# Kernel optimization log

Measured on AMD Instinct MI355X. Metric: run time of the kernel, lower is better.

The kernel has to match this reference:

```python
import jax, jax.numpy as jnp
import numpy as np

# Fixed query graph: 3 terms, 3 predicates, edges (head_term, tail_term, pred):
# (0,1,0), (1,2,1), (0,2,2) -> every term has degree 2 -> seq_len 3 incl. self.
T, P, B, D, H, NL, FF = 3, 3, 16384, 256, 8, 2, 1024
DH = D // H
SCALE = DH ** -0.5


def setup_inputs() -> dict:
    key = jax.random.key(0)
    ks = jax.random.split(key, 8)
    s = 0.02
    f = jnp.float32
    return {
        "term_embs": jax.random.normal(ks[0], (T, B, D), f),
        "pred_embs": jax.random.normal(ks[1], (P, B, D), f),
        "Wq": jax.random.normal(ks[2], (NL, D, D), f) * s,
        "Wk": jax.random.normal(ks[3], (NL, D, D), f) * s,
        "Wv": jax.random.normal(ks[4], (NL, D, D), f) * s,
        "Wo": jax.random.normal(ks[5], (NL, D, D), f) * s,
        "bq": jnp.zeros((NL, D), f),
        "bk": jnp.zeros((NL, D), f),
        "bv": jnp.zeros((NL, D), f),
        "bo": jnp.zeros((NL, D), f),
        "ln1_g": jnp.ones((NL, D), f),
        "ln1_b": jnp.zeros((NL, D), f),
        "ln2_g": jnp.ones((NL, D), f),
        "ln2_b": jnp.zeros((NL, D), f),
        "W1": jax.random.normal(ks[6], (NL, D, FF), f) * s,
        "b1": jnp.zeros((NL, FF), f),
        "W2": jax.random.normal(ks[7], (NL, FF, D), f) * s,
        "b2": jnp.zeros((NL, D), f),
        "lnf_g": jnp.ones((D,), f),
        "lnf_b": jnp.zeros((D,), f),
    }


def _layer_norm(x, g, b):
    m = jnp.mean(x, axis=-1, keepdims=True)
    v = jnp.var(x, axis=-1, keepdims=True)
    return (x - m) * jax.lax.rsqrt(v + 1e-5) * g + b


def _forward(term_embs, pred_embs, Wq, Wk, Wv, Wo, bq, bk, bv, bo,
             ln1_g, ln1_b, ln2_g, ln2_b, W1, b1, W2, b2, lnf_g, lnf_b):
    # --- message passing (TransE-style NBP): tail_est = head + pred, head_est = tail - pred
    # edge heads: [0,1,0], edge tails: [1,2,2]
    tail_msgs = term_embs[jnp.array([0, 1, 0])] + pred_embs  # [P,B,D] -> sent to tail terms
    head_msgs = term_embs[jnp.array([1, 2, 2])] - pred_embs  # [P,B,D] -> sent to head terms
    # collect per term (static gather) + self embedding appended last
    x0 = jnp.stack([head_msgs[0], head_msgs[2], term_embs[0]], axis=1)  # [B,3,D]
    x1 = jnp.stack([tail_msgs[0], head_msgs[1], term_embs[1]], axis=1)
    x2 = jnp.stack([tail_msgs[1], tail_msgs[2], term_embs[2]], axis=1)
    x = jnp.concatenate([x0, x1, x2], axis=0)  # [T*B, 3, D]
    # --- pre-norm Transformer encoder, NL layers (dropout off at eval)
    for l in range(NL):
        h = _layer_norm(x, ln1_g[l], ln1_b[l])
        q = (h @ Wq[l] + bq[l]).reshape(-1, 3, H, DH)
        k = (h @ Wk[l] + bk[l]).reshape(-1, 3, H, DH)
        v = (h @ Wv[l] + bv[l]).reshape(-1, 3, H, DH)
        a = jax.nn.softmax(jnp.einsum('nqhd,nkhd->nhqk', q, k) * SCALE, axis=-1)
        o = jnp.einsum('nhqk,nkhd->nqhd', a, v).reshape(-1, 3, D)
        x = x + o @ Wo[l] + bo[l]
        h = _layer_norm(x, ln2_g[l], ln2_b[l])
        x = x + jax.nn.relu(h @ W1[l] + b1[l]) @ W2[l] + b2[l]
    x = _layer_norm(x, lnf_g, lnf_b)
    # --- aggregate (agg_func='mean') over the small message sequence
    return jnp.mean(x, axis=1).reshape(T, B, D)


def reference(term_embs, pred_embs, Wq, Wk, Wv, Wo, bq, bk, bv, bo,
              ln1_g, ln1_b, ln2_g, ln2_b, W1, b1, W2, b2, lnf_g, lnf_b):
    return _forward(term_embs, pred_embs, Wq, Wk, Wv, Wo, bq, bk, bv, bo,
                    ln1_g, ln1_b, ln2_g, ln2_b, W1, b1, W2, b2, lnf_g, lnf_b)
```

## Files before the change

### kernel.cpp

```cpp
#include <hip/hip_runtime.h>
#include <hip/hip_bf16.h>
#include <stdint.h>

typedef __hip_bfloat16 bf16;
typedef unsigned short u16;
typedef unsigned int u32;
typedef __bf16 v8bf __attribute__((ext_vector_type(8)));
typedef float v4f __attribute__((ext_vector_type(4)));

#define NB 16384
#define MROWS 147456

__device__ __forceinline__ float b2f(u16 u) {
  union { u32 u; float f; } v; v.u = ((u32)u) << 16; return v.f;
}
__device__ __forceinline__ u16 f2b(float f) {
  union { float f; u32 u; } v; v.f = f;
  u32 u = v.u;
  return (u16)((u + 0x7fffu + ((u >> 16) & 1u)) >> 16);
}
__device__ __forceinline__ void async16(const u16* g, u16* lds) {
  __builtin_amdgcn_global_load_lds((const __attribute__((address_space(1))) void*)g,
                                   (__attribute__((address_space(3))) void*)lds,
                                   16, 0, 0);
}

__global__ __launch_bounds__(256)
void prep_weights(const float* Wq, const float* Wk, const float* Wv, const float* Wo,
                  const float* W1, const float* W2,
                  const float* bq, const float* bk, const float* bv,
                  bf16* wt, float* bqkv)
{
  if (blockIdx.x == 6144) {
    for (int e = threadIdx.x; e < 1536; e += 256) {
      int l = e / 768;
      int rem = e - l * 768;
      int wsel = rem >> 8;
      int col = rem & 255;
      const float* s = (wsel == 0) ? bq : (wsel == 1) ? bk : bv;
      bqkv[e] = s[l * 256 + col];
    }
    return;
  }
  int gid = blockIdx.x * 256 + threadIdx.x;
  int layer = (gid >= 786432) ? 1 : 0;
  int r = gid - layer * 786432;
  const float* src; int K, N, e, outoff;
  if (r < 262144) {
    int which = r >> 16;
    e = r & 65535; K = 256; N = 256;
    const float* w = (which == 0) ? Wq : (which == 1) ? Wk : (which == 2) ? Wv : Wo;
    src = w + layer * 65536;
    outoff = layer * 786432 + which * 65536;
  } else if (r < 524288) {
    e = r - 262144; K = 256; N = 1024;
    src = W1 + layer * 262144;
    outoff = layer * 786432 + 262144;
  } else {
    e = r - 524288; K = 1024; N = 256;
    src = W2 + layer * 262144;
    outoff = layer * 786432 + 524288;
  }
  int n = e / K, kk = e - n * K;
  ((u16*)wt)[outoff + e] = f2b(src[kk * N + n]);
}

__global__ __launch_bounds__(256)
void build_ln(const float* __restrict__ T, const float* __restrict__ P,
              const float* __restrict__ gp, const float* __restrict__ bp,
              float* __restrict__ X, bf16* __restrict__ H, int row0)
{
  const int lane = threadIdx.x & 63;
  const int lrow = blockIdx.x * 4 + (threadIdx.x >> 6);
  const int row = row0 + lrow;
  const int d0 = lane * 4;
  int n = row / 3;
  int t = row - n * 3;
  float4 v;
  if (t == 2) {
    v = *(const float4*)(T + (size_t)n * 256 + d0);
  } else {
    int tm = n >> 14, b = n & 16383;
    const int srcT[6] = {1, 2,  0, 2,  1, 0};
    const int srcP[6] = {0, 2,  0, 1,  1, 2};
    const float sg[6] = {-1.f, -1.f,  1.f, -1.f,  1.f, 1.f};
    int idx = tm * 2 + t;
    float4 tv = *(const float4*)(T + ((size_t)(srcT[idx] * NB + b)) * 256 + d0);
    float4 pv = *(const float4*)(P + ((size_t)(srcP[idx] * NB + b)) * 256 + d0);
    float s = sg[idx];
    v.x = tv.x + s * pv.x;
    v.y = tv.y + s * pv.y;
    v.z = tv.z + s * pv.z;
    v.w = tv.w + s * pv.w;
  }
  *(float4*)(X + (size_t)lrow * 256 + d0) = v;
  float s = v.x + v.y + v.z + v.w;
  float q = v.x * v.x + v.y * v.y + v.z * v.z + v.w * v.w;
  #pragma unroll
  for (int m = 32; m > 0; m >>= 1) {
    s += __shfl_xor(s, m, 64);
    q += __shfl_xor(q, m, 64);
  }
  float mean = s * (1.f / 256.f);
  float var = q * (1.f / 256.f) - mean * mean;
  float r = rsqrtf(var + 1e-5f);
  float4 gv = *(const float4*)(gp + d0);
  float4 bv = *(const float4*)(bp + d0);
  ushort4 outv;
  outv.x = f2b((v.x - mean) * r * gv.x + bv.x);
  outv.y = f2b((v.y - mean) * r * gv.y + bv.y);
  outv.z = f2b((v.z - mean) * r * gv.z + bv.z);
  outv.w = f2b((v.w - mean) * r * gv.w + bv.w);
  *(ushort4*)((u16*)H + (size_t)lrow * 256 + d0) = outv;
}

__global__ __launch_bounds__(256)
void ln_rows(const float* __restrict__ xp, const float* __restrict__ gp,
             const float* __restrict__ bp, bf16* __restrict__ hp)
{
  const int lane = threadIdx.x & 63;
  const int row = blockIdx.x * 4 + (threadIdx.x >> 6);
  float4 rv = *(const float4*)(xp + (size_t)row * 256 + lane * 4);
  float v0 = rv.x, v1 = rv.y, v2 = rv.z, v3 = rv.w;
  float s = v0 + v1 + v2 + v3;
  float q = v0 * v0 + v1 * v1 + v2 * v2 + v3 * v3;
  #pragma unroll
  for (int m = 32; m > 0; m >>= 1) {
    s += __shfl_xor(s, m, 64);
    q += __shfl_xor(q, m, 64);
  }
  float mean = s * (1.f / 256.f);
  float var = q * (1.f / 256.f) - mean * mean;
  float r = rsqrtf(var + 1e-5f);
  float4 gv = *(const float4*)(gp + lane * 4);
  float4 bv = *(const float4*)(bp + lane * 4);
  ushort4 outv;
  outv.x = f2b((v0 - mean) * r * gv.x + bv.x);
  outv.y = f2b((v1 - mean) * r * gv.y + bv.y);
  outv.z = f2b((v2 - mean) * r * gv.z + bv.z);
  outv.w = f2b((v3 - mean) * r * gv.w + bv.w);
  *(ushort4*)((u16*)hp + (size_t)row * 256 + lane * 4) = outv;
}

template<int RES, int RELU, int OUTF32>
__global__ __launch_bounds__(256)
void gemm_bt(const bf16* __restrict__ Ap, const bf16* __restrict__ Btp,
             const float* __restrict__ biasp, const float* __restrict__ resp,
             void* __restrict__ Cp, int N, int K,
             int btZ, int biasZ, long long cZ)
{
  __shared__ __align__(16) u16 As[2 * 128 * 32];
  __shared__ __align__(16) u16 Bs[2 * 128 * 32];
  const int z = blockIdx.z;
  const u16* A = (const u16*)Ap;
  const u16* Bt = (const u16*)Btp + (size_t)z * btZ;
  const float* bias = biasp + (size_t)z * biasZ;
  const int m0 = blockIdx.x * 128;
  const int n0 = blockIdx.y * 128;
  const int tid = threadIdx.x;
  const int w = tid >> 6, lane = tid & 63;
  const int waveM = (w & 1) * 64, waveN = (w >> 1) * 64;

  const int rrow = tid >> 2;
  const int kcol = (tid & 3) * 8;
  const u16* pA0 = A + (size_t)(m0 + rrow) * K + kcol;
  const u16* pA1 = A + (size_t)(m0 + rrow + 64) * K + kcol;
  const u16* pB0 = Bt + (size_t)(n0 + rrow) * K + kcol;
  const u16* pB1 = Bt + (size_t)(n0 + rrow + 64) * K + kcol;

  v4f acc[4][4];
  #pragma unroll
  for (int i = 0; i < 4; i++)
    #pragma unroll
    for (int j = 0; j < 4; j++) {
      v4f zz = {0.f, 0.f, 0.f, 0.f};
      acc[i][j] = zz;
    }

  const int rdA = (waveM + (lane & 15)) * 64 + (lane >> 4) * 16;
  const int rdB = (waveN + (lane & 15)) * 64 + (lane >> 4) * 16;
  const int nk = K >> 5;

  async16(pA0, As + w * 512);        async16(pA1, As + 2048 + w * 512);
  async16(pB0, Bs + w * 512);        async16(pB1, Bs + 2048 + w * 512);
  pA0 += 32; pA1 += 32; pB0 += 32; pB1 += 32;

  int cur = 0;
  for (int kt = 0; kt < nk; kt++) {
    __syncthreads();
    if (kt + 1 < nk) {
      const int nxt = (cur ^ 1) * 4096;
      async16(pA0, As + nxt + w * 512);        async16(pA1, As + nxt + 2048 + w * 512);
      async16(pB0, Bs + nxt + w * 512);        async16(pB1, Bs + nxt + 2048 + w * 512);
      pA0 += 32; pA1 += 32; pB0 += 32; pB1 += 32;
    }
    const char* AsC = (const char*)(As + cur * 4096);
    const char* BsC = (const char*)(Bs + cur * 4096);
    v8bf a[4], b[4];
    #pragma unroll
    for (int i = 0; i < 4; i++)
      a[i] = *(const v8bf*)(AsC + rdA + i * 1024);
    #pragma unroll
    for (int j = 0; j < 4; j++)
      b[j] = *(const v8bf*)(BsC + rdB + j * 1024);
    #pragma unroll
    for (int i = 0; i < 4; i++)
      #pragma unroll
      for (int j = 0; j < 4; j++)
        acc[i][j] = __builtin_amdgcn_mfma_f32_16x16x32_bf16(a[i], b[j], acc[i][j], 0, 0, 0);
    cur ^= 1;
  }

  float bv[4];
  #pragma unroll
  for (int j = 0; j < 4; j++)
    bv[j] = bias[n0 + waveN + j * 16 + (lane & 15)];

  #pragma unroll
  for (int i = 0; i < 4; i++) {
    #pragma unroll
    for (int r = 0; r < 4; r++) {
      int rowg = m0 + waveM + i * 16 + (lane >> 4) * 4 + r;
      size_t rb = (size_t)rowg * N;
      #pragma unroll
      for (int j = 0; j < 4; j++) {
        int colg = n0 + waveN + j * 16 + (lane & 15);
        float vv = acc[i][j][r] + bv[j];
        if (RES) vv += resp[rb + colg];
        if (RELU) vv = fmaxf(vv, 0.f);
        if (OUTF32) ((float*)Cp)[rb + colg] = vv;
        else ((u16*)Cp + (size_t)z * cZ)[rb + colg] = f2b(vv);
      }
    }
  }
}

__global__ __launch_bounds__(256)
void attn(const bf16* __restrict__ qp, const bf16* __restrict__ kp,
          const bf16* __restrict__ vp, bf16* __restrict__ op)
{
  __shared__ __align__(16) u16 qs[6144], ks[6144], vs[6144];
  __shared__ float probs[8][8][9];
  const int tid = threadIdx.x;
  const size_t gbase = (size_t)blockIdx.x * 6144;
  const uint4* qg = (const uint4*)((const u16*)qp + gbase);
  const uint4* kg = (const uint4*)((const u16*)kp + gbase);
  const uint4* vg = (const uint4*)((const u16*)vp + gbase);
  for (int c = tid; c < 768; c += 256) {
    ((uint4*)qs)[c] = qg[c];
    ((uint4*)ks)[c] = kg[c];
    ((uint4*)vs)[c] = vg[c];
  }
  __syncthreads();
  if (tid < 64) {
    int s = tid >> 3, h = tid & 7;
    int base = s * 768 + h * 32;
    float sc[3][3];
    #pragma unroll
    for (int i = 0; i < 3; i++)
      #pragma unroll
      for (int j = 0; j < 3; j++) {
        float sum = 0.f;
        #pragma unroll
        for (int d = 0; d < 32; d++)
          sum += b2f(qs[base + i * 256 + d]) * b2f(ks[base + j * 256 + d]);
        sc[i][j] = sum * 0.17677669529663687f;
      }
    #pragma unroll
    for (int i = 0; i < 3; i++) {
      float m = fmaxf(sc[i][0], fmaxf(sc[i][1], sc[i][2]));
      float e0 = __expf(sc[i][0] - m);
      float e1 = __expf(sc[i][1] - m);
      float e2 = __expf(sc[i][2] - m);
      float inv = 1.f / (e0 + e1 + e2);
      probs[s][h][i * 3 + 0] = e0 * inv;
      probs[s][h][i * 3 + 1] = e1 * inv;
      probs[s][h][i * 3 + 2] = e2 * inv;
    }
  }
  __syncthreads();
  u16* og = (u16*)op + gbase;
  for (int c = tid; c < 6144; c += 256) {
    int lrow = c >> 8, hd = c & 255;
    int s = lrow / 3, i = lrow - s * 3;
    int h = hd >> 5;
    float p0 = probs[s][h][i * 3 + 0];
    float p1 = probs[s][h][i * 3 + 1];
    float p2 = probs[s][h][i * 3 + 2];
    float o = p0 * b2f(vs[s * 768 + hd])
            + p1 * b2f(vs[s * 768 + 256 + hd])
            + p2 * b2f(vs[s * 768 + 512 + hd]);
    og[c] = f2b(o);
  }
}

__global__ __launch_bounds__(256)
void ln_final_mean(const float* __restrict__ xp, const float* __restrict__ gp,
                   const float* __restrict__ bp, float* __restrict__ outp)
{
  const int lane = threadIdx.x & 63;
  const int n = blockIdx.x * 4 + (threadIdx.x >> 6);
  float4 gv = *(const float4*)(gp + lane * 4);
  float4 bv4 = *(const float4*)(bp + lane * 4);
  float a0 = 0.f, a1 = 0.f, a2 = 0.f, a3 = 0.f;
  for (int t = 0; t < 3; t++) {
    float4 rv = *(const float4*)(xp + ((size_t)n * 3 + t) * 256 + lane * 4);
    float v0 = rv.x, v1 = rv.y, v2 = rv.z, v3 = rv.w;
    float s = v0 + v1 + v2 + v3;
    float q = v0 * v0 + v1 * v1 + v2 * v2 + v3 * v3;
    #pragma unroll
    for (int m = 32; m > 0; m >>= 1) {
      s += __shfl_xor(s, m, 64);
      q += __shfl_xor(q, m, 64);
    }
    float mean = s * (1.f / 256.f);
    float var = q * (1.f / 256.f) - mean * mean;
    float r = rsqrtf(var + 1e-5f);
    a0 += (v0 - mean) * r * gv.x + bv4.x;
    a1 += (v1 - mean) * r * gv.y + bv4.y;
    a2 += (v2 - mean) * r * gv.z + bv4.z;
    a3 += (v3 - mean) * r * gv.w + bv4.w;
  }
  const float third = 1.f / 3.f;
  float4 outv;
  outv.x = a0 * third;
  outv.y = a1 * third;
  outv.z = a2 * third;
  outv.w = a3 * third;
  *(float4*)(outp + (size_t)n * 256 + lane * 4) = outv;
}

extern "C" void kernel_launch(void* const* d_in, const int* in_sizes, int n_in,
                              void* d_out, int out_size, void* d_ws, size_t ws_size,
                              hipStream_t stream)
{
  const float* term = (const float*)d_in[0];
  const float* pred = (const float*)d_in[1];
  const float* Wq  = (const float*)d_in[2];
  const float* Wk  = (const float*)d_in[3];
  const float* Wv  = (const float*)d_in[4];
  const float* Wo  = (const float*)d_in[5];
  const float* bq  = (const float*)d_in[6];
  const float* bk  = (const float*)d_in[7];
  const float* bvv = (const float*)d_in[8];
  const float* bo  = (const float*)d_in[9];
  const float* ln1g = (const float*)d_in[10];
  const float* ln1b = (const float*)d_in[11];
  const float* ln2g = (const float*)d_in[12];
  const float* ln2b = (const float*)d_in[13];
  const float* W1  = (const float*)d_in[14];
  const float* b1  = (const float*)d_in[15];
  const float* W2  = (const float*)d_in[16];
  const float* b2  = (const float*)d_in[17];
  const float* lnfg = (const float*)d_in[18];
  const float* lnfb = (const float*)d_in[19];

  int nch = 128;
  for (int c = 1; c <= 128; c *= 2) {
    size_t Mc = (size_t)MROWS / c;
    size_t need = 4ull * 1024 * 1024 + Mc * 3584ull;
    if (need <= ws_size) { nch = c; break; }
  }
  const size_t Mc = (size_t)MROWS / nch;
  const int mBlocks = (int)(Mc / 128);

  char* ws = (char*)d_ws;
  bf16* wt   = (bf16*)ws;
  float* bqkv = (float*)(ws + 3145728);
  float* x = (float*)(ws + 4194304);
  bf16* h = (bf16*)(x + Mc * 256);
  bf16* q = h + Mc * 256;
  bf16* v_ = q + 2 * Mc * 256;
  bf16* o = q + 3 * Mc * 256;
  bf16* f = q;

  prep_weights<<<6145, 256, 0, stream>>>(Wq, Wk, Wv, Wo, W1, W2, bq, bk, bvv, wt, bqkv);

  const long long qkvZ = (long long)(Mc * 256);
  for (int ch = 0; ch < nch; ch++) {
    const int row0 = (int)(ch * Mc);
    build_ln<<<(int)(Mc / 4), 256, 0, stream>>>(term, pred, ln1g, ln1b, x, h, row0);
    for (int l = 0; l < 2; l++) {
      const bf16* wl = wt + l * 786432;
      if (l > 0)
        ln_rows<<<(int)(Mc / 4), 256, 0, stream>>>(x, ln1g + l * 256, ln1b + l * 256, h);
      gemm_bt<0, 0, 0><<<dim3(mBlocks, 2, 3), 256, 0, stream>>>(
          h, wl, bqkv + l * 768, nullptr, q, 256, 256, 65536, 256, qkvZ);
      attn<<<(int)(Mc / 24), 256, 0, stream>>>(q, q + Mc * 256, v_, o);
      gemm_bt<1, 0, 1><<<dim3(mBlocks, 2, 1), 256, 0, stream>>>(
          o, wl + 196608, bo + l * 256, x, x, 256, 256, 0, 0, 0);
      ln_rows<<<(int)(Mc / 4), 256, 0, stream>>>(x, ln2g + l * 256, ln2b + l * 256, h);
      gemm_bt<0, 1, 0><<<dim3(mBlocks, 8, 1), 256, 0, stream>>>(
          h, wl + 262144, b1 + l * 1024, nullptr, f, 1024, 256, 0, 0, 0);
      gemm_bt<1, 0, 1><<<dim3(mBlocks, 2, 1), 256, 0, stream>>>(
          f, wl + 524288, b2 + l * 256, x, x, 256, 1024, 0, 0, 0);
    }
    ln_final_mean<<<(int)(Mc / 12), 256, 0, stream>>>(
        x, lnfg, lnfb, (float*)d_out + (size_t)(row0 / 3) * 256);
  }
}
```

Measured before the change: 1.594 ms.

## Fuse layernorm into QKV and FFN GEMMs with row-resident LDS tiles

Replaces the generic tiled GEMM plus separate layernorm launches with specialized kernels. LN1 is folded into the QKV projection and LN2 into the FFN, where the 1024-wide hidden activation stays in LDS chunk by chunk instead of round-tripping through global memory. Each block keeps a 64x256 swizzled A tile in LDS and reads weight fragments directly from global/L2. This cuts activation traffic and launch count, but B operands are no longer staged in LDS, the QKV weights are re-read per block, and the chunk-count search now starts at 4.

```diff
diff --git a/kernel.cpp b/kernel.cpp
--- a/kernel.cpp
+++ b/kernel.cpp
@@ -23,6 +23,19 @@
   __builtin_amdgcn_global_load_lds((const __attribute__((address_space(1))) void*)g,
                                    (__attribute__((address_space(3))) void*)lds,
                                    16, 0, 0);
+}
+__device__ __forceinline__ v4f mfma16(v8bf a, v8bf b, v4f c) {
+  return __builtin_amdgcn_mfma_f32_16x16x32_bf16(a, b, c, 0, 0, 0);
+}
+__device__ __forceinline__ v8bf ldsA256(const u16* As, int row, int k) {
+  int byte = (row << 9) + (k << 1);
+  byte ^= (row & 7) << 4;
+  return *(const v8bf*)((const char*)As + byte);
+}
+__device__ __forceinline__ v8bf ldsA128(const u16* As, int row, int k) {
+  int byte = (row << 8) + (k << 1);
+  byte ^= (row & 7) << 4;
+  return *(const v8bf*)((const char*)As + byte);
 }
 
 __global__ __launch_bounds__(256)
@@ -66,9 +79,8 @@
 }
 
 __global__ __launch_bounds__(256)
-void build_ln(const float* __restrict__ T, const float* __restrict__ P,
-              const float* __restrict__ gp, const float* __restrict__ bp,
-              float* __restrict__ X, bf16* __restrict__ H, int row0)
+void build_x(const float* __restrict__ T, const float* __restrict__ P,
+             float* __restrict__ X, int row0)
 {
   const int lane = threadIdx.x & 63;
   const int lrow = blockIdx.x * 4 + (threadIdx.x >> 6);
@@ -94,144 +106,237 @@
     v.w = tv.w + s * pv.w;
   }
   *(float4*)(X + (size_t)lrow * 256 + d0) = v;
-  float s = v.x + v.y + v.z + v.w;
-  float q = v.x * v.x + v.y * v.y + v.z * v.z + v.w * v.w;
-  #pragma unroll
-  for (int m = 32; m > 0; m >>= 1) {
-    s += __shfl_xor(s, m, 64);
-    q += __shfl_xor(q, m, 64);
-  }
-  float mean = s * (1.f / 256.f);
-  float var = q * (1.f / 256.f) - mean * mean;
-  float r = rsqrtf(var + 1e-5f);
-  float4 gv = *(const float4*)(gp + d0);
-  float4 bv = *(const float4*)(bp + d0);
-  ushort4 outv;
-  outv.x = f2b((v.x - mean) * r * gv.x + bv.x);
-  outv.y = f2b((v.y - mean) * r * gv.y + bv.y);
-  outv.z = f2b((v.z - mean) * r * gv.z + bv.z);
-  outv.w = f2b((v.w - mean) * r * gv.w + bv.w);
-  *(ushort4*)((u16*)H + (size_t)lrow * 256 + d0) = outv;
-}
-
-__global__ __launch_bounds__(256)
-void ln_rows(const float* __restrict__ xp, const float* __restrict__ gp,
-             const float* __restrict__ bp, bf16* __restrict__ hp)
-{
-  const int lane = threadIdx.x & 63;
-  const int row = blockIdx.x * 4 + (threadIdx.x >> 6);
-  float4 rv = *(const float4*)(xp + (size_t)row * 256 + lane * 4);
-  float v0 = rv.x, v1 = rv.y, v2 = rv.z, v3 = rv.w;
-  float s = v0 + v1 + v2 + v3;
-  float q = v0 * v0 + v1 * v1 + v2 * v2 + v3 * v3;
-  #pragma unroll
-  for (int m = 32; m > 0; m >>= 1) {
-    s += __shfl_xor(s, m, 64);
-    q += __shfl_xor(q, m, 64);
-  }
-  float mean = s * (1.f / 256.f);
-  float var = q * (1.f / 256.f) - mean * mean;
-  float r = rsqrtf(var + 1e-5f);
-  float4 gv = *(const float4*)(gp + lane * 4);
-  float4 bv = *(const float4*)(bp + lane * 4);
-  ushort4 outv;
-  outv.x = f2b((v0 - mean) * r * gv.x + bv.x);
-  outv.y = f2b((v1 - mean) * r * gv.y + bv.y);
-  outv.z = f2b((v2 - mean) * r * gv.z + bv.z);
-  outv.w = f2b((v3 - mean) * r * gv.w + bv.w);
-  *(ushort4*)((u16*)hp + (size_t)row * 256 + lane * 4) = outv;
-}
-
-template<int RES, int RELU, int OUTF32>
-__global__ __launch_bounds__(256)
-void gemm_bt(const bf16* __restrict__ Ap, const bf16* __restrict__ Btp,
-             const float* __restrict__ biasp, const float* __restrict__ resp,
-             void* __restrict__ Cp, int N, int K,
-             int btZ, int biasZ, long long cZ)
-{
-  __shared__ __align__(16) u16 As[2 * 128 * 32];
-  __shared__ __align__(16) u16 Bs[2 * 128 * 32];
-  const int z = blockIdx.z;
-  const u16* A = (const u16*)Ap;
-  const u16* Bt = (const u16*)Btp + (size_t)z * btZ;
-  const float* bias = biasp + (size_t)z * biasZ;
-  const int m0 = blockIdx.x * 128;
-  const int n0 = blockIdx.y * 128;
+}
+
+__device__ __forceinline__ void ln_stage(const float* __restrict__ xp,
+                                         const float* __restrict__ gp,
+                                         const float* __restrict__ bp,
+                                         u16* As, int m0, int w, int lane)
+{
+  const float4 gv = *(const float4*)(gp + lane * 4);
+  const float4 bv = *(const float4*)(bp + lane * 4);
+  for (int r = w; r < 64; r += 8) {
+    float4 v = *(const float4*)(xp + (size_t)(m0 + r) * 256 + lane * 4);
+    float s = v.x + v.y + v.z + v.w;
+    float q = v.x * v.x + v.y * v.y + v.z * v.z + v.w * v.w;
+    #pragma unroll
+    for (int m = 32; m > 0; m >>= 1) {
+      s += __shfl_xor(s, m, 64);
+      q += __shfl_xor(q, m, 64);
+    }
+    float mean = s * (1.f / 256.f);
+    float var = q * (1.f / 256.f) - mean * mean;
+    float rr = rsqrtf(var + 1e-5f);
+    ushort4 o;
+    o.x = f2b((v.x - mean) * rr * gv.x + bv.x);
+    o.y = f2b((v.y - mean) * rr * gv.y + bv.y);
+    o.z = f2b((v.z - mean) * rr * gv.z + bv.z);
+    o.w = f2b((v.w - mean) * rr * gv.w + bv.w);
+    int byte = (r << 9) + (lane << 3);
+    byte ^= (r & 7) << 4;
+    *(ushort4*)((char*)As + byte) = o;
+  }
+}
+
+__global__ __launch_bounds__(512, 4)
+void qkv_fused(const float* __restrict__ xp, const float* __restrict__ gp,
+               const float* __restrict__ bp, const bf16* __restrict__ wp,
+               const float* __restrict__ biasp, bf16* __restrict__ qkv,
+               long long qkvZ)
+{
+  __shared__ __align__(16) u16 As[64 * 256];
   const int tid = threadIdx.x;
   const int w = tid >> 6, lane = tid & 63;
-  const int waveM = (w & 1) * 64, waveN = (w >> 1) * 64;
-
-  const int rrow = tid >> 2;
-  const int kcol = (tid & 3) * 8;
-  const u16* pA0 = A + (size_t)(m0 + rrow) * K + kcol;
-  const u16* pA1 = A + (size_t)(m0 + rrow + 64) * K + kcol;
-  const u16* pB0 = Bt + (size_t)(n0 + rrow) * K + kcol;
-  const u16* pB1 = Bt + (size_t)(n0 + rrow + 64) * K + kcol;
-
-  v4f acc[4][4];
-  #pragma unroll
-  for (int i = 0; i < 4; i++)
+  const int m0 = blockIdx.x * 64;
+  ln_stage(xp, gp, bp, As, m0, w, lane);
+  __syncthreads();
+  const int wr = (w >> 2) * 32;
+  const int wc = (w & 3) * 32;
+  const int fl = lane & 15, fh = lane >> 4;
+  #pragma unroll 1
+  for (int nb = 0; nb < 6; nb++) {
+    const int wsel = nb >> 1, c0 = (nb & 1) * 128;
+    const u16* B = (const u16*)wp + wsel * 65536 + (size_t)(c0 + wc) * 256;
+    v4f acc[2][2];
+    #pragma unroll
+    for (int i = 0; i < 2; i++)
+      #pragma unroll
+      for (int j = 0; j < 2; j++) {
+        v4f z = {0.f, 0.f, 0.f, 0.f};
+        acc[i][j] = z;
+      }
+    #pragma unroll
+    for (int kk = 0; kk < 8; kk++) {
+      const int k0 = kk * 32 + fh * 8;
+      v8bf a0 = ldsA256(As, wr + fl, k0);
+      v8bf a1 = ldsA256(As, wr + 16 + fl, k0);
+      v8bf b0 = *(const v8bf*)(B + (size_t)fl * 256 + k0);
+      v8bf b1 = *(const v8bf*)(B + (size_t)(16 + fl) * 256 + k0);
+      acc[0][0] = mfma16(a0, b0, acc[0][0]);
+      acc[1][0] = mfma16(a1, b0, acc[1][0]);
+      acc[0][1] = mfma16(a0, b1, acc[0][1]);
+      acc[1][1] = mfma16(a1, b1, acc[1][1]);
+    }
+    u16* out = (u16*)qkv + (size_t)wsel * qkvZ;
+    #pragma unroll
+    for (int nj = 0; nj < 2; nj++) {
+      const int col = c0 + wc + nj * 16 + fl;
+      const float bb = biasp[wsel * 256 + col];
+      #pragma unroll
+      for (int mi = 0; mi < 2; mi++)
+        #pragma unroll
+        for (int r2 = 0; r2 < 4; r2++) {
+          int row = m0 + wr + mi * 16 + fh * 4 + r2;
+          out[(size_t)row * 256 + col] = f2b(acc[mi][nj][r2] + bb);
+        }
+    }
+  }
+}
+
+__global__ __launch_bounds__(512, 4)
+void oproj(const bf16* __restrict__ op, const bf16* __restrict__ wop,
+           const float* __restrict__ bop, float* __restrict__ xp)
+{
+  __shared__ __align__(16) u16 As[64 * 256];
+  const int tid = threadIdx.x;
+  const int w = tid >> 6, lane = tid & 63;
+  const int m0 = blockIdx.x * 64;
+  const u16* og = (const u16*)op + (size_t)m0 * 256;
+  #pragma unroll
+  for (int i = 0; i < 4; i++) {
+    int b = i * 8192 + tid * 16;
+    int row = b >> 9, cb = b & 511;
+    int srfranja = (row << 8) + ((cb ^ ((row & 7) << 4)) >> 1);
+    async16(og + srfranja, As + (b >> 1));
+  }
+  __syncthreads();
+  const int wr = (w >> 2) * 32;
+  const int wc = (w & 3) * 64;
+  const int fl = lane & 15, fh = lane >> 4;
+  v4f acc[2][4];
+  #pragma unroll
+  for (int i = 0; i < 2; i++)
     #pragma unroll
     for (int j = 0; j < 4; j++) {
-      v4f zz = {0.f, 0.f, 0.f, 0.f};
-      acc[i][j] = zz;
-    }
-
-  const int rdA = (waveM + (lane & 15)) * 64 + (lane >> 4) * 16;
-  const int rdB = (waveN + (lane & 15)) * 64 + (lane >> 4) * 16;
-  const int nk = K >> 5;
-
-  async16(pA0, As + w * 512);        async16(pA1, As + 2048 + w * 512);
-  async16(pB0, Bs + w * 512);        async16(pB1, Bs + 2048 + w * 512);
-  pA0 += 32; pA1 += 32; pB0 += 32; pB1 += 32;
-
-  int cur = 0;
-  for (int kt = 0; kt < nk; kt++) {
+      v4f z = {0.f, 0.f, 0.f, 0.f};
+      acc[i][j] = z;
+    }
+  #pragma unroll
+  for (int kk = 0; kk < 8; kk++) {
+    const int k0 = kk * 32 + fh * 8;
+    v8bf a0 = ldsA256(As, wr + fl, k0);
+    v8bf a1 = ldsA256(As, wr + 16 + fl, k0);
+    #pragma unroll
+    for (int nj = 0; nj < 4; nj++) {
+      v8bf b = *(const v8bf*)((const u16*)wop + (size_t)(wc + nj * 16 + fl) * 256 + k0);
+      acc[0][nj] = mfma16(a0, b, acc[0][nj]);
+      acc[1][nj] = mfma16(a1, b, acc[1][nj]);
+    }
+  }
+  #pragma unroll
+  for (int nj = 0; nj < 4; nj++) {
+    const int col = wc + nj * 16 + fl;
+    const float bb = bop[col];
+    #pragma unroll
+    for (int mi = 0; mi < 2; mi++)
+      #pragma unroll
+      for (int r2 = 0; r2 < 4; r2++) {
+        size_t idx = (size_t)(m0 + wr + mi * 16 + fh * 4 + r2) * 256 + col;
+        xp[idx] += acc[mi][nj][r2] + bb;
+      }
+  }
+}
+
+__global__ __launch_bounds__(512, 4)
+void ffn_fused(float* __restrict__ xp, const float* __restrict__ gp,
+               const float* __restrict__ bp, const bf16* __restrict__ w1p,
+               const bf16* __restrict__ w2p, const float* __restrict__ b1p,
+               const float* __restrict__ b2p)
+{
+  __shared__ __align__(16) u16 As[64 * 256];
+  __shared__ __align__(16) u16 Fs[64 * 128];
+  const int tid = threadIdx.x;
+  const int w = tid >> 6, lane = tid & 63;
+  const int m0 = blockIdx.x * 64;
+  ln_stage(xp, gp, bp, As, m0, w, lane);
+  __syncthreads();
+  const int wr = (w >> 2) * 32;
+  const int wc = (w & 3);
+  const int fl = lane & 15, fh = lane >> 4;
+  v4f acc[2][4];
+  #pragma unroll
+  for (int i = 0; i < 2; i++)
+    #pragma unroll
+    for (int j = 0; j < 4; j++) {
+      v4f z = {0.f, 0.f, 0.f, 0.f};
+      acc[i][j] = z;
+    }
+  #pragma unroll 1
+  for (int nc = 0; nc < 8; nc++) {
+    v4f fa[2][2];
+    #pragma unroll
+    for (int i = 0; i < 2; i++)
+      #pragma unroll
+      for (int j = 0; j < 2; j++) {
+        v4f z = {0.f, 0.f, 0.f, 0.f};
+        fa[i][j] = z;
+      }
+    const u16* B1 = (const u16*)w1p + (size_t)(nc * 128 + wc * 32) * 256;
+    #pragma unroll
+    for (int kk = 0; kk < 8; kk++) {
+      const int k0 = kk * 32 + fh * 8;
+      v8bf a0 = ldsA256(As, wr + fl, k0);
+      v8bf a1 = ldsA256(As, wr + 16 + fl, k0);
+      v8bf b0 = *(const v8bf*)(B1 + (size_t)fl * 256 + k0);
+      v8bf b1 = *(const v8bf*)(B1 + (size_t)(16 + fl) * 256 + k0);
+      fa[0][0] = mfma16(a0, b0, fa[0][0]);
+      fa[1][0] = mfma16(a1, b0, fa[1][0]);
+      fa[0][1] = mfma16(a0, b1, fa[0][1]);
+      fa[1][1] = mfma16(a1, b1, fa[1][1]);
+    }
+    #pragma unroll
+    for (int nj = 0; nj < 2; nj++) {
+      const int colc = wc * 32 + nj * 16 + fl;
+      const float bb = b1p[nc * 128 + colc];
+      #pragma unroll
+      for (int mi = 0; mi < 2; mi++)
+        #pragma unroll
+        for (int r2 = 0; r2 < 4; r2++) {
+          int row = wr + mi * 16 + fh * 4 + r2;
+          float vv = fmaxf(fa[mi][nj][r2] + bb, 0.f);
+          int byte = (row << 8) + (colc << 1);
+          byte ^= (row & 7) << 4;
+          *(u16*)((char*)Fs + byte) = f2b(vv);
+        }
+    }
     __syncthreads();
-    if (kt + 1 < nk) {
-      const int nxt = (cur ^ 1) * 4096;
-      async16(pA0, As + nxt + w * 512);        async16(pA1, As + nxt + 2048 + w * 512);
-      async16(pB0, Bs + nxt + w * 512);        async16(pB1, Bs + nxt + 2048 + w * 512);
-      pA0 += 32; pA1 += 32; pB0 += 32; pB1 += 32;
-    }
-    const char* AsC = (const char*)(As + cur * 4096);
-    const char* BsC = (const char*)(Bs + cur * 4096);
-    v8bf a[4], b[4];
-    #pragma unroll
-    for (int i = 0; i < 4; i++)
-      a[i] = *(const v8bf*)(AsC + rdA + i * 1024);
-    #pragma unroll
-    for (int j = 0; j < 4; j++)
-      b[j] = *(const v8bf*)(BsC + rdB + j * 1024);
-    #pragma unroll
-    for (int i = 0; i < 4; i++)
-      #pragma unroll
-      for (int j = 0; j < 4; j++)
-        acc[i][j] = __builtin_amdgcn_mfma_f32_16x16x32_bf16(a[i], b[j], acc[i][j], 0, 0, 0);
-    cur ^= 1;
-  }
-
-  float bv[4];
-  #pragma unroll
-  for (int j = 0; j < 4; j++)
-    bv[j] = bias[n0 + waveN + j * 16 + (lane & 15)];
-
-  #pragma unroll
-  for (int i = 0; i < 4; i++) {
-    #pragma unroll
-    for (int r = 0; r < 4; r++) {
-      int rowg = m0 + waveM + i * 16 + (lane >> 4) * 4 + r;
-      size_t rb = (size_t)rowg * N;
-      #pragma unroll
-      for (int j = 0; j < 4; j++) {
-        int colg = n0 + waveN + j * 16 + (lane & 15);
-        float vv = acc[i][j][r] + bv[j];
-        if (RES) vv += resp[rb + colg];
-        if (RELU) vv = fmaxf(vv, 0.f);
-        if (OUTF32) ((float*)Cp)[rb + colg] = vv;
-        else ((u16*)Cp + (size_t)z * cZ)[rb + colg] = f2b(vv);
-      }
-    }
+    #pragma unroll
+    for (int kk = 0; kk < 4; kk++) {
+      const int k0 = kk * 32 + fh * 8;
+      v8bf a0 = ldsA128(Fs, wr + fl, k0);
+      v8bf a1 = ldsA128(Fs, wr + 16 + fl, k0);
+      #pragma unroll
+      for (int nj = 0; nj < 4; nj++) {
+        v8bf b = *(const v8bf*)((const u16*)w2p +
+                                (size_t)((w & 3) * 64 + nj * 16 + fl) * 1024 +
+                                nc * 128 + k0);
+        acc[0][nj] = mfma16(a0, b, acc[0][nj]);
+        acc[1][nj] = mfma16(a1, b, acc[1][nj]);
+      }
+    }
+    __syncthreads();
+  }
+  #pragma unroll
+  for (int nj = 0; nj < 4; nj++) {
+    const int col = (w & 3) * 64 + nj * 16 + fl;
+    const float bb = b2p[col];
+    #pragma unroll
+    for (int mi = 0; mi < 2; mi++)
+      #pragma unroll
+      for (int r2 = 0; r2 < 4; r2++) {
+        size_t idx = (size_t)(m0 + wr + mi * 16 + fh * 4 + r2) * 256 + col;
+        xp[idx] += acc[mi][nj][r2] + bb;
+      }
   }
 }
 
@@ -356,44 +461,36 @@
   const float* lnfb = (const float*)d_in[19];
 
   int nch = 128;
-  for (int c = 1; c <= 128; c *= 2) {
-    size_t Mc = (size_t)MROWS / c;
-    size_t need = 4ull * 1024 * 1024 + Mc * 3584ull;
+  for (int c = 4; c <= 128; c *= 2) {
+    size_t Mc_ = (size_t)MROWS / c;
+    size_t need = 4ull * 1024 * 1024 + Mc_ * 3072ull;
     if (need <= ws_size) { nch = c; break; }
   }
   const size_t Mc = (size_t)MROWS / nch;
-  const int mBlocks = (int)(Mc / 128);
 
   char* ws = (char*)d_ws;
   bf16* wt   = (bf16*)ws;
   float* bqkv = (float*)(ws + 3145728);
   float* x = (float*)(ws + 4194304);
-  bf16* h = (bf16*)(x + Mc * 256);
-  bf16* q = h + Mc * 256;
+  bf16* q = (bf16*)(x + Mc * 256);
   bf16* v_ = q + 2 * Mc * 256;
   bf16* o = q + 3 * Mc * 256;
-  bf16* f = q;
 
   prep_weights<<<6145, 256, 0, stream>>>(Wq, Wk, Wv, Wo, W1, W2, bq, bk, bvv, wt, bqkv);
 
   const long long qkvZ = (long long)(Mc * 256);
   for (int ch = 0; ch < nch; ch++) {
     const int row0 = (int)(ch * Mc);
-    build_ln<<<(int)(Mc / 4), 256, 0, stream>>>(term, pred, ln1g, ln1b, x, h, row0);
+    build_x<<<(int)(Mc / 4), 256, 0, stream>>>(term, pred, x, row0);
     for (int l = 0; l < 2; l++) {
-      const bf16* wl = wt + l * 786432;
-      if (l > 0)
-        ln_rows<<<(int)(Mc / 4), 256, 0, stream>>>(x, ln1g + l * 256, ln1b + l * 256, h);
-      gemm_bt<0, 0, 0><<<dim3(mBlocks, 2, 3), 256, 0, stream>>>(
-          h, wl, bqkv + l * 768, nullptr, q, 256, 256, 65536, 256, qkvZ);
+      const bf16* wl = wt + (size_t)l * 786432;
+      qkv_fused<<<(int)(Mc / 64), 512, 0, stream>>>(
+          x, ln1g + l * 256, ln1b + l * 256, wl, bqkv + l * 768, q, qkvZ);
       attn<<<(int)(Mc / 24), 256, 0, stream>>>(q, q + Mc * 256, v_, o);
-      gemm_bt<1, 0, 1><<<dim3(mBlocks, 2, 1), 256, 0, stream>>>(
-          o, wl + 196608, bo + l * 256, x, x, 256, 256, 0, 0, 0);
-      ln_rows<<<(int)(Mc / 4), 256, 0, stream>>>(x, ln2g + l * 256, ln2b + l * 256, h);
-      gemm_bt<0, 1, 0><<<dim3(mBlocks, 8, 1), 256, 0, stream>>>(
-          h, wl + 262144, b1 + l * 1024, nullptr, f, 1024, 256, 0, 0, 0);
-      gemm_bt<1, 0, 1><<<dim3(mBlocks, 2, 1), 256, 0, stream>>>(
-          f, wl + 524288, b2 + l * 256, x, x, 256, 1024, 0, 0, 0);
+      oproj<<<(int)(Mc / 64), 512, 0, stream>>>(o, wl + 196608, bo + l * 256, x);
+      ffn_fused<<<(int)(Mc / 64), 512, 0, stream>>>(
+          x, ln2g + l * 256, ln2b + l * 256, wl + 262144, wl + 524288,
+          b1 + l * 1024, b2 + l * 256);
     }
     ln_final_mean<<<(int)(Mc / 12), 256, 0, stream>>>(
         x, lnfg, lnfb, (float*)d_out + (size_t)(row0 / 3) * 256);
```

Result: slower. 2.904 ms (+82.2%).

## Swizzle GEMM LDS layout, remap blocks across XCDs, raise occupancy hint

Applied to the files above, without the earlier changes.

The GEMM kernel now uses a 1D grid. Block IDs are remapped so that consecutive work tiles, which share the same A rows across N and z tiles, land on the same XCD (bid&7 interleave), improving L2 reuse of the A panel. The LDS tile layout is XOR-swizzled on the 16-byte chunk index, both for the async global-to-LDS writes and for the MFMA fragment reads, to reduce bank conflicts. launch_bounds is raised to 4 blocks per CU, which may constrain registers. The remap assumes the grid size is divisible by 8.

```diff
diff --git a/kernel.cpp b/kernel.cpp
--- a/kernel.cpp
+++ b/kernel.cpp
@@ -143,26 +143,33 @@
 }
 
 template<int RES, int RELU, int OUTF32>
-__global__ __launch_bounds__(256)
+__global__ __launch_bounds__(256, 4)
 void gemm_bt(const bf16* __restrict__ Ap, const bf16* __restrict__ Btp,
              const float* __restrict__ biasp, const float* __restrict__ resp,
              void* __restrict__ Cp, int N, int K,
-             int btZ, int biasZ, long long cZ)
+             int btZ, int biasZ, long long cZ, int nB, int nz)
 {
   __shared__ __align__(16) u16 As[2 * 128 * 32];
   __shared__ __align__(16) u16 Bs[2 * 128 * 32];
-  const int z = blockIdx.z;
+  const int per = gridDim.x >> 3;
+  const int bid = blockIdx.x;
+  const int work = (bid & 7) * per + (bid >> 3);
+  const int m = work / nz;
+  const int rwk = work - m * nz;
+  const int n = rwk % nB;
+  const int z = rwk / nB;
+
   const u16* A = (const u16*)Ap;
   const u16* Bt = (const u16*)Btp + (size_t)z * btZ;
   const float* bias = biasp + (size_t)z * biasZ;
-  const int m0 = blockIdx.x * 128;
-  const int n0 = blockIdx.y * 128;
+  const int m0 = m * 128;
+  const int n0 = n * 128;
   const int tid = threadIdx.x;
   const int w = tid >> 6, lane = tid & 63;
   const int waveM = (w & 1) * 64, waveN = (w >> 1) * 64;
 
   const int rrow = tid >> 2;
-  const int kcol = (tid & 3) * 8;
+  const int kcol = ((tid & 3) ^ ((rrow >> 1) & 3)) * 8;
   const u16* pA0 = A + (size_t)(m0 + rrow) * K + kcol;
   const u16* pA1 = A + (size_t)(m0 + rrow + 64) * K + kcol;
   const u16* pB0 = Bt + (size_t)(n0 + rrow) * K + kcol;
@@ -177,8 +184,10 @@
       acc[i][j] = zz;
     }
 
-  const int rdA = (waveM + (lane & 15)) * 64 + (lane >> 4) * 16;
-  const int rdB = (waveN + (lane & 15)) * 64 + (lane >> 4) * 16;
+  const int rowA = waveM + (lane & 15);
+  const int rdA = rowA * 64 + ((((lane >> 4) ^ ((rowA >> 1) & 3))) << 4);
+  const int rowB = waveN + (lane & 15);
+  const int rdB = rowB * 64 + ((((lane >> 4) ^ ((rowB >> 1) & 3))) << 4);
   const int nk = K >> 5;
 
   async16(pA0, As + w * 512);        async16(pA1, As + 2048 + w * 512);
@@ -357,12 +366,12 @@
 
   int nch = 128;
   for (int c = 1; c <= 128; c *= 2) {
-    size_t Mc = (size_t)MROWS / c;
-    size_t need = 4ull * 1024 * 1024 + Mc * 3584ull;
+    size_t Mc_ = (size_t)MROWS / c;
+    size_t need = 4ull * 1024 * 1024 + Mc_ * 3584ull;
     if (need <= ws_size) { nch = c; break; }
   }
   const size_t Mc = (size_t)MROWS / nch;
-  const int mBlocks = (int)(Mc / 128);
+  const int mB = (int)(Mc / 128);
 
   char* ws = (char*)d_ws;
   bf16* wt   = (bf16*)ws;
@@ -381,19 +390,19 @@
     const int row0 = (int)(ch * Mc);
     build_ln<<<(int)(Mc / 4), 256, 0, stream>>>(term, pred, ln1g, ln1b, x, h, row0);
     for (int l = 0; l < 2; l++) {
-      const bf16* wl = wt + l * 786432;
+      const bf16* wl = wt + (size_t)l * 786432;
       if (l > 0)
         ln_rows<<<(int)(Mc / 4), 256, 0, stream>>>(x, ln1g + l * 256, ln1b + l * 256, h);
-      gemm_bt<0, 0, 0><<<dim3(mBlocks, 2, 3), 256, 0, stream>>>(
-          h, wl, bqkv + l * 768, nullptr, q, 256, 256, 65536, 256, qkvZ);
+      gemm_bt<0, 0, 0><<<mB * 6, 256, 0, stream>>>(
+          h, wl, bqkv + l * 768, nullptr, q, 256, 256, 65536, 256, qkvZ, 2, 6);
       attn<<<(int)(Mc / 24), 256, 0, stream>>>(q, q + Mc * 256, v_, o);
-      gemm_bt<1, 0, 1><<<dim3(mBlocks, 2, 1), 256, 0, stream>>>(
-          o, wl + 196608, bo + l * 256, x, x, 256, 256, 0, 0, 0);
+      gemm_bt<1, 0, 1><<<mB * 2, 256, 0, stream>>>(
+          o, wl + 196608, bo + l * 256, x, x, 256, 256, 0, 0, 0, 2, 2);
       ln_rows<<<(int)(Mc / 4), 256, 0, stream>>>(x, ln2g + l * 256, ln2b + l * 256, h);
-      gemm_bt<0, 1, 0><<<dim3(mBlocks, 8, 1), 256, 0, stream>>>(
-          h, wl + 262144, b1 + l * 1024, nullptr, f, 1024, 256, 0, 0, 0);
-      gemm_bt<1, 0, 1><<<dim3(mBlocks, 2, 1), 256, 0, stream>>>(
-          f, wl + 524288, b2 + l * 256, x, x, 256, 1024, 0, 0, 0);
+      gemm_bt<0, 1, 0><<<mB * 8, 256, 0, stream>>>(
+          h, wl + 262144, b1 + l * 1024, nullptr, f, 1024, 256, 0, 0, 0, 8, 8);
+      gemm_bt<1, 0, 1><<<mB * 2, 256, 0, stream>>>(
+          f, wl + 524288, b2 + l * 256, x, x, 256, 1024, 0, 0, 0, 2, 2);
     }
     ln_final_mean<<<(int)(Mc / 12), 256, 0, stream>>>(
         x, lnfg, lnfb, (float*)d_out + (size_t)(row0 / 3) * 256);
```

Measured after the change: 1.330 ms. -16.6%, faster.
